# Kernel tuning notes

Measured on AMD Instinct MI355X. Metric: run time of the kernel, lower is better.

Reference implementation:

```python
import jax, jax.numpy as jnp
import numpy as np
import math

EMBED_DIM = 512
NUM_HEADS = 8
NUM_EXPERTS = 16
TOP_K = 8
B, T = 2, 1024


def setup_inputs() -> dict:
    key = jax.random.key(0)
    ks = jax.random.split(key, 16)
    d, E = EMBED_DIM, NUM_EXPERTS
    hdim = 4 * d  # expert hidden width
    s = 0.02
    inp = {
        "x": jax.random.normal(ks[0], (B, T, d), jnp.float32),
        # RMSNorm params (init ones, matching torch module)
        "g": jnp.ones((d,), jnp.float32),
        "b": jnp.ones((d,), jnp.float32),
        # attention
        "c_attn_w": jax.random.normal(ks[1], (d, 3 * d), jnp.float32) * s,
        "c_attn_b": jnp.zeros((3 * d,), jnp.float32),
        "alpha": jnp.ones((NUM_HEADS,), jnp.float32),
        "c_proj_w": jax.random.normal(ks[2], (d, d), jnp.float32) * s,
        "c_proj_b": jnp.zeros((d,), jnp.float32),
        # router
        "router_w": jax.random.normal(ks[3], (d, E), jnp.float32) * s,
        "router_b": jnp.zeros((E,), jnp.float32),
        # stacked expert params: Linear(d,4d) -> SwiGLU(4d,4d) -> Linear(4d,d)
        "w_in": jax.random.normal(ks[4], (E, d, hdim), jnp.float32) * s,
        "b_in": jnp.zeros((E, hdim), jnp.float32),
        "w1": jax.random.normal(ks[5], (E, hdim, 2 * hdim), jnp.float32) * s,
        "b1": jnp.zeros((E, 2 * hdim), jnp.float32),
        "w2": jax.random.normal(ks[6], (E, hdim, hdim), jnp.float32) * s,
        "b2": jnp.zeros((E, hdim), jnp.float32),
        "w_out": jax.random.normal(ks[7], (E, hdim, d), jnp.float32) * s,
        "b_out": jnp.zeros((E, d), jnp.float32),
    }
    return inp


def _block(x, g, b, c_attn_w, c_attn_b, alpha, c_proj_w, c_proj_b,
           router_w, router_b, w_in, b_in, w1, b1, w2, b2, w_out, b_out):
    Bb, Tt, C = x.shape
    H = alpha.shape[0]
    hd = C // H
    E = router_b.shape[0]

    # RMSNorm (note: additive b, per original module)
    rms = jnp.sqrt(jnp.mean(x * x, axis=-1, keepdims=True) + 1e-6)
    xn = (x / rms) * g + b

    # QK-normalized causal attention
    qkv = xn @ c_attn_w + c_attn_b                      # [B,T,3C]
    q, k, v = jnp.split(qkv, 3, axis=-1)
    def heads(t):
        return t.reshape(Bb, Tt, H, hd).transpose(0, 2, 1, 3)  # [B,H,T,hd]
    q, k, v = heads(q), heads(k), heads(v)
    eps = 1e-5
    q_hat = q / (jnp.linalg.norm(q, axis=-1, keepdims=True) + eps)
    k_hat = k / (jnp.linalg.norm(k, axis=-1, keepdims=True) + eps)
    factor = (alpha * math.sqrt(hd)).reshape(1, H, 1, 1)
    q_scaled = q_hat * factor
    # SDPA default scale = 1/sqrt(head_dim)
    scores = jnp.einsum("bhqd,bhkd->bhqk", q_scaled, k_hat) / math.sqrt(hd)
    causal = jnp.tril(jnp.ones((Tt, Tt), bool))
    scores = jnp.where(causal, scores, -jnp.inf)
    att = jax.nn.softmax(scores, axis=-1)
    y = jnp.einsum("bhqk,bhkd->bhqd", att, v)
    y = y.transpose(0, 2, 1, 3).reshape(Bb, Tt, C)
    y = y @ c_proj_w + c_proj_b
    x = x + y

    # Router + top-8 normalized gates
    routes = jax.nn.softmax(x @ router_w + router_b, axis=-1)  # [B,T,E]
    probs, idx = jax.lax.top_k(routes, TOP_K)
    probs = probs / jnp.sum(probs, axis=-1, keepdims=True)
    # combine weights per expert: [B,T,E]
    gates = jnp.sum(jax.nn.one_hot(idx, E, dtype=x.dtype) * probs[..., None], axis=2)

    # Dense expert evaluation (faithful math: unselected tokens get zero gate)
    N = Bb * Tt
    xf = x.reshape(N, C)
    gf = gates.reshape(N, E)
    h = jnp.einsum("nd,edf->enf", xf, w_in) + b_in[:, None, :]      # [E,N,4d]
    c = jnp.einsum("enf,efg->eng", h, w1) + b1[:, None, :]          # [E,N,8d]
    a, bb2 = jnp.split(c, 2, axis=-1)
    s = (bb2 * jax.nn.sigmoid(bb2)) * a                              # SwiGLU
    o = jnp.einsum("enf,efg->eng", s, w2) + b2[:, None, :]          # [E,N,4d]
    eo = jnp.einsum("enf,efd->end", o, w_out) + b_out[:, None, :]   # [E,N,d]
    moe = jnp.einsum("end,ne->nd", eo, gf).reshape(Bb, Tt, C)
    return x + moe


def reference(x, g, b, c_attn_w, c_attn_b, alpha, c_proj_w, c_proj_b,
              router_w, router_b, w_in, b_in, w1, b1, w2, b2, w_out, b_out):
    return _block(x, g, b, c_attn_w, c_attn_b, alpha, c_proj_w, c_proj_b,
                  router_w, router_b, w_in, b_in, w1, b1, w2, b2, w_out, b_out)
```

## Files before the change

kernel.cpp:

```cpp
#include <hip/hip_runtime.h>
#include <stdint.h>

#define DEVI __device__ __forceinline__
#define FENCE() asm volatile("" ::: "memory")

typedef short short8 __attribute__((ext_vector_type(8)));
typedef short short4v __attribute__((ext_vector_type(4)));
typedef float f32x4 __attribute__((ext_vector_type(4)));

DEVI float bf2f(unsigned short s){ union{unsigned u; float f;} x; x.u = ((unsigned)s)<<16; return x.f; }
DEVI unsigned short f2bf(float f){ union{float f; unsigned u;} x; x.f=f; unsigned r = x.u + 0x7fff + ((x.u>>16)&1); return (unsigned short)(r>>16); }

DEVI void gload_lds16(const void* g, void* l){
  __builtin_amdgcn_global_load_lds((const __attribute__((address_space(1))) unsigned int*)g,
                                   (__attribute__((address_space(3))) unsigned int*)l, 16, 0, 0);
}

__global__ __launch_bounds__(256)
void transpose_cvt(const float* __restrict__ in, unsigned short* __restrict__ out, int K, int N)
{
  __shared__ float tile[32][33];
  size_t zoff = (size_t)blockIdx.z * K * N;
  const float* src = in + zoff;
  unsigned short* dst = out + zoff;
  int kb = blockIdx.y*32, nb = blockIdx.x*32;
  int t = threadIdx.x;
  int tr = t>>3, tc = (t&7)*4;
  float4 v = *(const float4*)(src + (size_t)(kb+tr)*N + nb + tc);
  tile[tr][tc+0]=v.x; tile[tr][tc+1]=v.y; tile[tr][tc+2]=v.z; tile[tr][tc+3]=v.w;
  __syncthreads();
  short4v ov;
  ov[0] = (short)f2bf(tile[tc+0][tr]);
  ov[1] = (short)f2bf(tile[tc+1][tr]);
  ov[2] = (short)f2bf(tile[tc+2][tr]);
  ov[3] = (short)f2bf(tile[tc+3][tr]);
  *(short4v*)(dst + (size_t)(nb+tr)*K + kb + tc) = ov;
}

__global__ __launch_bounds__(256)
void rmsnorm_k(const float* __restrict__ x, const float* __restrict__ gw,
               const float* __restrict__ bw, unsigned short* __restrict__ xn)
{
  int row = blockIdx.x*4 + (threadIdx.x>>6);
  int lane = threadIdx.x & 63;
  const float* xr = x + (size_t)row*512 + lane*8;
  float4 a = *(const float4*)xr;
  float4 c = *(const float4*)(xr+4);
  float ss = a.x*a.x+a.y*a.y+a.z*a.z+a.w*a.w + c.x*c.x+c.y*c.y+c.z*c.z+c.w*c.w;
  #pragma unroll
  for (int m=1;m<64;m<<=1) ss += __shfl_xor(ss, m);
  float inv = 1.0f / sqrtf(ss*(1.f/512.f) + 1e-6f);
  const float* gr = gw + lane*8; const float* br = bw + lane*8;
  float4 g0=*(const float4*)gr, g1=*(const float4*)(gr+4);
  float4 b0=*(const float4*)br, b1=*(const float4*)(br+4);
  short8 o;
  o[0]=(short)f2bf(a.x*inv*g0.x + b0.x);
  o[1]=(short)f2bf(a.y*inv*g0.y + b0.y);
  o[2]=(short)f2bf(a.z*inv*g0.z + b0.z);
  o[3]=(short)f2bf(a.w*inv*g0.w + b0.w);
  o[4]=(short)f2bf(c.x*inv*g1.x + b1.x);
  o[5]=(short)f2bf(c.y*inv*g1.y + b1.y);
  o[6]=(short)f2bf(c.z*inv*g1.z + b1.z);
  o[7]=(short)f2bf(c.w*inv*g1.w + b1.w);
  *(short8*)(xn + (size_t)row*512 + lane*8) = o;
}

template<int EPI>
__global__ __launch_bounds__(512, 2)
void gemm3(const unsigned short* __restrict__ A, const unsigned short* __restrict__ B,
           const float* __restrict__ bias,
           float* __restrict__ Cf, unsigned short* __restrict__ Ch,
           const unsigned short* __restrict__ aux,
           int M, int N, int K,
           const int* __restrict__ off, long long strideBz, long long strideBiasz)
{
  __shared__ char smem[147456];
  int z = blockIdx.z;
  int rowbase = 0, Mz = M;
  if (off){ rowbase = off[z]; Mz = off[z+1] - rowbase; }
  int row0 = blockIdx.y * 256;
  if (row0 >= Mz) return;
  int col0 = blockIdx.x * 128;
  const unsigned short* Ab = A + (size_t)(rowbase + row0) * K;
  const unsigned short* Bb = B + (size_t)z * strideBz + (size_t)col0 * K;
  const float* biasz = bias + (size_t)z * strideBiasz;

  int tid = threadIdx.x;
  int lane = tid & 63, w = tid >> 6;
  int lrow = lane & 15, lg = lane >> 4;
  int wr = w >> 1, wc = w & 1;

  f32x4 acc[4][4];
  #pragma unroll
  for (int i=0;i<4;i++){
    #pragma unroll
    for (int j=0;j<4;j++) acc[i][j] = f32x4{0.f,0.f,0.f,0.f};
  }

  int nkt = K >> 6;

  auto stage = [&](int kt2, int part){
    if (kt2 >= nkt) return;
    char* sA = smem + (kt2 % 3) * 49152;
    char* sB = sA + 32768;
    int k0 = kt2 << 6;
    #pragma unroll
    for (int i=0;i<2;i++){
      int s = (part*2 + i)*512 + tid;
      int r = s >> 3, kb = (s & 7) ^ (r & 7);
      gload_lds16(Ab + (size_t)r*K + k0 + kb*8, sA + s*16);
    }
    {
      int s = part*512 + tid;
      int r = s >> 3, kb = (s & 7) ^ (r & 7);
      gload_lds16(Bb + (size_t)r*K + k0 + kb*8, sB + s*16);
    }
  };

  stage(0,0); stage(0,1); stage(1,0); stage(1,1);
  asm volatile("s_waitcnt vmcnt(6)" ::: "memory");
  __builtin_amdgcn_s_barrier();
  FENCE();

  for (int kt = 0; kt < nkt; kt++){
    char* sA = smem + (kt % 3) * 49152;
    char* sB = sA + 32768;
    short8 bfr[4][2], afr[4][2];
    #pragma unroll
    for (int n=0;n<4;n++){
      int ct = wc*64 + n*16 + lrow;
      #pragma unroll
      for (int kk=0;kk<2;kk++){
        int kbb = lg + kk*4;
        bfr[n][kk] = *(const short8*)(sB + ct*128 + ((kbb ^ (ct&7))<<4));
      }
    }
    #pragma unroll
    for (int m=0;m<2;m++){
      int rt = wr*64 + m*16 + lrow;
      #pragma unroll
      for (int kk=0;kk<2;kk++){
        int kbb = lg + kk*4;
        afr[m][kk] = *(const short8*)(sA + rt*128 + ((kbb ^ (rt&7))<<4));
      }
    }
    stage(kt+2, 0);
    FENCE(); __builtin_amdgcn_s_barrier(); FENCE();
    __builtin_amdgcn_s_setprio(1);
    #pragma unroll
    for (int m=0;m<2;m++){
      #pragma unroll
      for (int n=0;n<4;n++){
        #pragma unroll
        for (int kk=0;kk<2;kk++)
          acc[m][n] = __builtin_amdgcn_mfma_f32_16x16x32_bf16(afr[m][kk], bfr[n][kk], acc[m][n], 0,0,0);
      }
    }
    __builtin_amdgcn_s_setprio(0);
    FENCE(); __builtin_amdgcn_s_barrier(); FENCE();
    #pragma unroll
    for (int m=2;m<4;m++){
      int rt = wr*64 + m*16 + lrow;
      #pragma unroll
      for (int kk=0;kk<2;kk++){
        int kbb = lg + kk*4;
        afr[m][kk] = *(const short8*)(sA + rt*128 + ((kbb ^ (rt&7))<<4));
      }
    }
    stage(kt+2, 1);
    FENCE(); __builtin_amdgcn_s_barrier(); FENCE();
    __builtin_amdgcn_s_setprio(1);
    #pragma unroll
    for (int m=2;m<4;m++){
      #pragma unroll
      for (int n=0;n<4;n++){
        #pragma unroll
        for (int kk=0;kk<2;kk++)
          acc[m][n] = __builtin_amdgcn_mfma_f32_16x16x32_bf16(afr[m][kk], bfr[n][kk], acc[m][n], 0,0,0);
      }
    }
    __builtin_amdgcn_s_setprio(0);
    asm volatile("s_waitcnt vmcnt(6)" ::: "memory");
    FENCE(); __builtin_amdgcn_s_barrier(); FENCE();
  }

  #pragma unroll
  for (int m=0;m<4;m++){
    int rloc = wr*64 + m*16 + lg*4;
    #pragma unroll
    for (int j=0;j<4;j++){
      int row = row0 + rloc + j;
      if (row < Mz){
        size_t rg = (size_t)(rowbase + row);
        #pragma unroll
        for (int n=0;n<4;n++){
          int col = col0 + wc*64 + n*16 + lrow;
          float v = acc[m][n][j] + biasz[col];
          size_t idx = rg * N + col;
          if constexpr (EPI == 0){
            Cf[idx] = v;
          } else if constexpr (EPI == 1){
            Ch[idx] = f2bf(v);
          } else {
            float a = bf2f(aux[idx]);
            float sg = v / (1.f + __expf(-v));
            Ch[idx] = f2bf(a * sg);
          }
        }
      }
    }
  }
}

__global__ __launch_bounds__(256)
void gemm_proj(const unsigned short* __restrict__ A, const unsigned short* __restrict__ B,
               const float* __restrict__ bias,
               float* __restrict__ Cf, unsigned short* __restrict__ Ch,
               const float* __restrict__ resid, int M, int N, int K)
{
  __shared__ char smem[32768];
  char* smA = smem; char* smB = smem + 16384;
  int row0 = blockIdx.y * 128;
  int col0 = blockIdx.x * 128;
  int t = threadIdx.x, w = t>>6, lane = t&63;
  int lrow = lane&15, lg = lane>>4;
  int wr = w>>1, wc = w&1;

  f32x4 acc[4][4];
  #pragma unroll
  for (int i=0;i<4;i++){
    #pragma unroll
    for (int j=0;j<4;j++) acc[i][j] = f32x4{0.f,0.f,0.f,0.f};
  }
  const size_t Abase = (size_t)row0 * K;
  const size_t Bbase = (size_t)col0 * K;
  int nkt = K >> 6;
  for (int kt=0; kt<nkt; kt++){
    __syncthreads();
    int k0 = kt*64;
    #pragma unroll
    for (int i=0;i<4;i++){
      int s = (i*4 + w)*64 + lane;
      int r = s>>3;
      int kb = (s&7) ^ (r&7);
      gload_lds16(A + Abase + (size_t)r*K + k0 + kb*8, smA + (size_t)(i*4+w)*1024);
      gload_lds16(B + Bbase + (size_t)r*K + k0 + kb*8, smB + (size_t)(i*4+w)*1024);
    }
    __syncthreads();
    #pragma unroll
    for (int ks=0; ks<2; ks++){
      short8 af[4], bf[4];
      int kbb = lg + ks*4;
      #pragma unroll
      for (int m=0;m<4;m++){
        int rt = wr*64 + m*16 + lrow;
        af[m] = *(const short8*)(smA + rt*128 + ((kbb ^ (rt&7))<<4));
      }
      #pragma unroll
      for (int n=0;n<4;n++){
        int rt = wc*64 + n*16 + lrow;
        bf[n] = *(const short8*)(smB + rt*128 + ((kbb ^ (rt&7))<<4));
      }
      #pragma unroll
      for (int m=0;m<4;m++){
        #pragma unroll
        for (int n=0;n<4;n++)
          acc[m][n] = __builtin_amdgcn_mfma_f32_16x16x32_bf16(af[m], bf[n], acc[m][n], 0,0,0);
      }
    }
  }
  #pragma unroll
  for (int m=0;m<4;m++){
    int rloc = wr*64 + m*16 + lg*4;
    #pragma unroll
    for (int j=0;j<4;j++){
      int row = row0 + rloc + j;
      size_t rg = (size_t)row;
      #pragma unroll
      for (int n=0;n<4;n++){
        int col = col0 + wc*64 + n*16 + lrow;
        float v = acc[m][n][j] + bias[col];
        size_t idx = rg * N + col;
        v += resid[idx];
        Cf[idx] = v;
        Ch[idx] = f2bf(v);
      }
    }
  }
}

__global__ __launch_bounds__(256)
void prep_qkv(const float* __restrict__ qkv, const float* __restrict__ alpha,
              unsigned short* __restrict__ q_s, unsigned short* __restrict__ k_hat,
              unsigned short* __restrict__ v_t)
{
  int idx = blockIdx.x*4 + (threadIdx.x>>6);
  int lane = threadIdx.x & 63;
  int h = idx & 7, bt = idx >> 3;
  size_t base = (size_t)bt*1536 + h*64 + lane;
  float qv = qkv[base], kv = qkv[base+512], vv = qkv[base+1024];
  float qs2 = qv*qv, ks2 = kv*kv;
  #pragma unroll
  for (int m=1;m<64;m<<=1){ qs2 += __shfl_xor(qs2, m); ks2 += __shfl_xor(ks2, m); }
  float qh = qv / (sqrtf(qs2) + 1e-5f) * alpha[h];
  float kh = kv / (sqrtf(ks2) + 1e-5f);
  int b = bt >> 10, tt = bt & 1023;
  size_t hb = ((size_t)(b*8+h))*1024*64;
  q_s[hb + (size_t)tt*64 + lane] = f2bf(qh);
  k_hat[hb + (size_t)tt*64 + lane] = f2bf(kh);
  v_t[((size_t)(b*8+h)*64 + lane)*1024 + tt] = f2bf(vv);
}

__global__ __launch_bounds__(256)
void attn_k(const unsigned short* __restrict__ q_s, const unsigned short* __restrict__ k_hat,
            const unsigned short* __restrict__ v_t, unsigned short* __restrict__ y)
{
  __shared__ char sm[51200];
  char* smK = sm + 18432;
  char* smV = sm + 34816;
  int qt = blockIdx.x, bh = blockIdx.y;
  int b = bh>>3, h = bh&7;
  int t = threadIdx.x, w = t>>6, lane = t&63;
  int lrow = lane&15, lg = lane>>4;
  int q0 = qt*128;
  const size_t hQK = (size_t)bh*1024*64;
  const size_t hV  = (size_t)bh*64*1024;

  #pragma unroll
  for (int i=0;i<4;i++){
    int s = (i*4+w)*64 + lane;
    int r = s>>3, kb = (s&7)^(r&7);
    gload_lds16(q_s + hQK + (size_t)(q0+r)*64 + kb*8, sm + (size_t)(i*4+w)*1024);
  }
  __syncthreads();
  short8 qf[2][2];
  #pragma unroll
  for (int mf=0;mf<2;mf++){
    #pragma unroll
    for (int ks=0;ks<2;ks++){
      int rt = w*32 + mf*16 + lrow;
      int kbb = lg + ks*4;
      qf[mf][ks] = *(const short8*)(sm + rt*128 + ((kbb^(rt&7))<<4));
    }
  }
  f32x4 oacc[2][4];
  #pragma unroll
  for (int i=0;i<2;i++){
    #pragma unroll
    for (int j=0;j<4;j++) oacc[i][j] = f32x4{0.f,0.f,0.f,0.f};
  }
  float mrun[2][4], lrun[2][4];
  #pragma unroll
  for (int i=0;i<2;i++){
    #pragma unroll
    for (int j=0;j<4;j++){ mrun[i][j] = -1e30f; lrun[i][j] = 0.f; }
  }
  char* Pw = sm + w*4608;

  for (int kt=0; kt<=qt; kt++){
    __syncthreads();
    int t0 = kt*128;
    #pragma unroll
    for (int i=0;i<4;i++){
      int s = (i*4+w)*64 + lane;
      int r = s>>3, kb = (s&7)^(r&7);
      gload_lds16(k_hat + hQK + (size_t)(t0+r)*64 + kb*8, smK + (size_t)(i*4+w)*1024);
    }
    #pragma unroll
    for (int i=0;i<4;i++){
      int s = (i*4+w)*64 + lane;
      int d = s>>4, kb2 = s&15;
      int kb = kb2 ^ (d&7);
      gload_lds16(v_t + hV + (size_t)d*1024 + t0 + kb*8, smV + (size_t)(i*4+w)*1024);
    }
    __syncthreads();

    f32x4 sacc[2][8];
    #pragma unroll
    for (int i=0;i<2;i++){
      #pragma unroll
      for (int j=0;j<8;j++) sacc[i][j] = f32x4{0.f,0.f,0.f,0.f};
    }
    #pragma unroll
    for (int ks=0;ks<2;ks++){
      short8 kf[8];
      int kbb = lg + ks*4;
      #pragma unroll
      for (int nf=0;nf<8;nf++){
        int rt = nf*16+lrow;
        kf[nf] = *(const short8*)(smK + rt*128 + ((kbb^(rt&7))<<4));
      }
      #pragma unroll
      for (int mf=0;mf<2;mf++){
        #pragma unroll
        for (int nf=0;nf<8;nf++)
          sacc[mf][nf] = __builtin_amdgcn_mfma_f32_16x16x32_bf16(qf[mf][ks], kf[nf], sacc[mf][nf], 0,0,0);
      }
    }
    if (kt == qt){
      #pragma unroll
      for (int mf=0;mf<2;mf++){
        #pragma unroll
        for (int nf=0;nf<8;nf++){
          #pragma unroll
          for (int j=0;j<4;j++){
            int qi = w*32+mf*16+lg*4+j;
            int ki = nf*16 + lrow;
            if (ki > qi) sacc[mf][nf][j] = -1e30f;
          }
        }
      }
    }
    #pragma unroll
    for (int mf=0;mf<2;mf++){
      #pragma unroll
      for (int j=0;j<4;j++){
        float mx = sacc[mf][0][j];
        #pragma unroll
        for (int nf=1;nf<8;nf++) mx = fmaxf(mx, sacc[mf][nf][j]);
        #pragma unroll
        for (int m=1;m<16;m<<=1) mx = fmaxf(mx, __shfl_xor(mx, m));
        float mnew = fmaxf(mrun[mf][j], mx);
        float sc = __expf(mrun[mf][j] - mnew);
        float rs = 0.f;
        #pragma unroll
        for (int nf=0;nf<8;nf++){
          float p = __expf(sacc[mf][nf][j] - mnew);
          sacc[mf][nf][j] = p; rs += p;
        }
        #pragma unroll
        for (int m=1;m<16;m<<=1) rs += __shfl_xor(rs, m);
        lrun[mf][j] = lrun[mf][j]*sc + rs;
        mrun[mf][j] = mnew;
        #pragma unroll
        for (int n2=0;n2<4;n2++) oacc[mf][n2][j] *= sc;
      }
    }
    #pragma unroll
    for (int half=0; half<2; half++){
      #pragma unroll
      for (int mf=0;mf<2;mf++){
        #pragma unroll
        for (int nfh=0;nfh<4;nfh++){
          int nf = half*4 + nfh;
          #pragma unroll
          for (int j=0;j<4;j++){
            int row = mf*16 + lg*4 + j;
            int col = nfh*16 + lrow;
            *(unsigned short*)(Pw + (row*72 + col)*2) = f2bf(sacc[mf][nf][j]);
          }
        }
      }
      #pragma unroll
      for (int k2=0;k2<2;k2++){
        int ks2 = half*2 + k2;
        short8 pf[2], vf[4];
        #pragma unroll
        for (int mf=0;mf<2;mf++)
          pf[mf] = *(const short8*)(Pw + (mf*16+lrow)*144 + lg*16 + k2*64);
        #pragma unroll
        for (int n2=0;n2<4;n2++){
          int d = n2*16+lrow;
          int kbb2 = lg + ks2*4;
          vf[n2] = *(const short8*)(smV + d*256 + ((kbb2^(d&7))<<4));
        }
        #pragma unroll
        for (int mf=0;mf<2;mf++){
          #pragma unroll
          for (int n2=0;n2<4;n2++)
            oacc[mf][n2] = __builtin_amdgcn_mfma_f32_16x16x32_bf16(pf[mf], vf[n2], oacc[mf][n2], 0,0,0);
        }
      }
    }
  }
  #pragma unroll
  for (int mf=0;mf<2;mf++){
    #pragma unroll
    for (int n2=0;n2<4;n2++){
      #pragma unroll
      for (int j=0;j<4;j++){
        float v = oacc[mf][n2][j] / lrun[mf][j];
        int qi = q0 + w*32 + mf*16 + lg*4 + j;
        int d = n2*16 + lrow;
        y[((size_t)(b*1024+qi))*512 + h*64 + d] = f2bf(v);
      }
    }
  }
}

__global__ __launch_bounds__(256)
void router_topk(const float* __restrict__ x2f, const float* __restrict__ rw,
                 const float* __restrict__ rb, float* __restrict__ gates)
{
  int tkn = blockIdx.x*4 + (threadIdx.x>>6);
  int lane = threadIdx.x & 63;
  int e = lane & 15, p = lane >> 4;
  const float* xr = x2f + (size_t)tkn*512;
  float part = 0.f;
  for (int d = p*128; d < p*128+128; d++)
    part += xr[d] * rw[d*16 + e];
  part += __shfl_xor(part, 16);
  part += __shfl_xor(part, 32);
  float logit = part + rb[e];
  float mx = logit;
  #pragma unroll
  for (int m=1;m<16;m<<=1) mx = fmaxf(mx, __shfl_xor(mx, m));
  float ex = __expf(logit - mx);
  float sm = ex;
  #pragma unroll
  for (int m=1;m<16;m<<=1) sm += __shfl_xor(sm, m);
  float prob = ex / sm;
  bool taken = false;
  float ssum = 0.f;
  #pragma unroll
  for (int r=0;r<8;r++){
    float cv = taken ? -1.f : prob;
    int ci = e;
    #pragma unroll
    for (int m=1;m<16;m<<=1){
      float ov = __shfl_xor(cv, m);
      int oi = __shfl_xor(ci, m);
      if (ov > cv || (ov == cv && oi < ci)){ cv = ov; ci = oi; }
    }
    if (e == ci) taken = true;
    ssum += cv;
  }
  if (lane < 16)
    gates[(size_t)tkn*16 + e] = taken ? prob / ssum : 0.f;
}

__global__ void listbuild(const float* __restrict__ gates, int* __restrict__ list,
                          int* __restrict__ slot, int* __restrict__ cnt)
{
  int e = blockIdx.x;
  int tid = threadIdx.x, w = tid>>6, lane = tid&63;
  __shared__ int sbase;
  __shared__ int wsum[4];
  if (tid==0) sbase = 0;
  __syncthreads();
  for (int c=0;c<8;c++){
    int tk = c*256 + tid;
    bool flag = gates[(size_t)tk*16 + e] > 0.f;
    unsigned long long bal = __ballot(flag);
    if (lane==0) wsum[w] = (int)__popcll(bal);
    __syncthreads();
    int wpref = 0;
    for (int i=0;i<w;i++) wpref += wsum[i];
    int tot = wsum[0]+wsum[1]+wsum[2]+wsum[3];
    int lpref = (int)__popcll(bal & ((1ull<<lane)-1ull));
    if (flag){
      int pos = sbase + wpref + lpref;
      list[e*2048 + pos] = tk;
      slot[(size_t)tk*16 + e] = pos;
    }
    __syncthreads();
    if (tid==0) sbase += tot;
    __syncthreads();
  }
  if (tid==0) cnt[e] = sbase;
}

__global__ void prefix_off(const int* __restrict__ cnt, int* __restrict__ off){
  if (threadIdx.x==0 && blockIdx.x==0){
    int a=0;
    for (int e=0;e<16;e++){ off[e]=a; a+=cnt[e]; }
    off[16]=a;
  }
}

__global__ __launch_bounds__(256)
void gather_rows(const unsigned short* __restrict__ x2h, const int* __restrict__ list,
                 const int* __restrict__ cnt, const int* __restrict__ off,
                 unsigned short* __restrict__ xe)
{
  int e = blockIdx.y;
  int s = blockIdx.x*4 + (threadIdx.x>>6);
  if (s >= cnt[e]) return;
  int lane = threadIdx.x & 63;
  int tk = list[e*2048 + s];
  *(short8*)(xe + ((size_t)(off[e]+s))*512 + lane*8) =
      *(const short8*)(x2h + (size_t)tk*512 + lane*8);
}

__global__ __launch_bounds__(256)
void combine_k(const float* __restrict__ x2f, const unsigned short* __restrict__ eo,
               const float* __restrict__ gates, const int* __restrict__ slot,
               const int* __restrict__ off, float* __restrict__ out)
{
  int tkn = blockIdx.x;
  __shared__ float gs[16];
  __shared__ int rws[16];
  int tid = threadIdx.x;
  if (tid < 16){
    float g = gates[(size_t)tkn*16 + tid];
    gs[tid] = g;
    rws[tid] = (g > 0.f) ? (off[tid] + slot[(size_t)tkn*16 + tid]) : 0;
  }
  __syncthreads();
  for (int d = tid; d < 512; d += 256){
    float v = x2f[(size_t)tkn*512 + d];
    #pragma unroll
    for (int e=0;e<16;e++){
      float g = gs[e];
      if (g > 0.f) v += g * bf2f(eo[(size_t)rws[e]*512 + d]);
    }
    out[(size_t)tkn*512 + d] = v;
  }
}

extern "C" void kernel_launch(void* const* d_in, const int* in_sizes, int n_in,
                              void* d_out, int out_size, void* d_ws, size_t ws_size,
                              hipStream_t stream) {
  (void)in_sizes; (void)n_in; (void)out_size; (void)ws_size;
  const float* x    = (const float*)d_in[0];
  const float* gw   = (const float*)d_in[1];
  const float* bw   = (const float*)d_in[2];
  const float* caw  = (const float*)d_in[3];
  const float* cab  = (const float*)d_in[4];
  const float* alpha= (const float*)d_in[5];
  const float* cpw  = (const float*)d_in[6];
  const float* cpb  = (const float*)d_in[7];
  const float* rw   = (const float*)d_in[8];
  const float* rb   = (const float*)d_in[9];
  const float* w_in = (const float*)d_in[10];
  const float* b_in = (const float*)d_in[11];
  const float* w1   = (const float*)d_in[12];
  const float* b1   = (const float*)d_in[13];
  const float* w2   = (const float*)d_in[14];
  const float* b2   = (const float*)d_in[15];
  const float* w_out= (const float*)d_in[16];
  const float* b_out= (const float*)d_in[17];

  char* ws = (char*)d_ws;
  size_t o = 0;
  auto alloc = [&](size_t bytes)->char*{
    char* p = ws + o;
    o += (bytes + 255) & ~(size_t)255;
    return p;
  };
  const size_t PADROWS = 16896;
  unsigned short* wT_attn = (unsigned short*)alloc(1536ull*512*2);
  unsigned short* wT_proj = (unsigned short*)alloc(512ull*512*2);
  unsigned short* wT_in   = (unsigned short*)alloc(16ull*2048*512*2);
  unsigned short* wT_1    = (unsigned short*)alloc(16ull*4096*2048*2);
  unsigned short* wT_2    = (unsigned short*)alloc(16ull*2048*2048*2);
  unsigned short* wT_out  = (unsigned short*)alloc(16ull*512*2048*2);
  unsigned short* xn      = (unsigned short*)alloc(2048ull*512*2);
  float*          qkv     = (float*)alloc(2048ull*1536*4);
  unsigned short* q_s     = (unsigned short*)alloc(2048ull*512*2);
  unsigned short* k_hat   = (unsigned short*)alloc(2048ull*512*2);
  unsigned short* v_t     = (unsigned short*)alloc(2048ull*512*2);
  unsigned short* ybuf    = (unsigned short*)alloc(2048ull*512*2);
  float*          x2f     = (float*)alloc(2048ull*512*4);
  unsigned short* x2h     = (unsigned short*)alloc(2048ull*512*2);
  float*          gates   = (float*)alloc(2048ull*16*4);
  int*            slot    = (int*)alloc(2048ull*16*4);
  int*            list    = (int*)alloc(16ull*2048*4);
  int*            cnt     = (int*)alloc(64);
  int*            off     = (int*)alloc(256);
  unsigned short* xe      = (unsigned short*)alloc(PADROWS*512*2);
  unsigned short* hbuf    = (unsigned short*)alloc(PADROWS*2048*2);
  unsigned short* c1buf   = (unsigned short*)alloc(PADROWS*2048*2);
  unsigned short* sbuf    = (unsigned short*)alloc(PADROWS*2048*2);
  unsigned short* eobuf   = xe;
  unsigned short* obuf    = hbuf;

  dim3 blk(256);
  dim3 blk5(512);
  transpose_cvt<<<dim3(1536/32, 512/32, 1), blk, 0, stream>>>(caw, wT_attn, 512, 1536);
  transpose_cvt<<<dim3(512/32, 512/32, 1), blk, 0, stream>>>(cpw, wT_proj, 512, 512);
  transpose_cvt<<<dim3(2048/32, 512/32, 16), blk, 0, stream>>>(w_in, wT_in, 512, 2048);
  transpose_cvt<<<dim3(4096/32, 2048/32, 16), blk, 0, stream>>>(w1, wT_1, 2048, 4096);
  transpose_cvt<<<dim3(2048/32, 2048/32, 16), blk, 0, stream>>>(w2, wT_2, 2048, 2048);
  transpose_cvt<<<dim3(512/32, 2048/32, 16), blk, 0, stream>>>(w_out, wT_out, 2048, 512);

  rmsnorm_k<<<512, blk, 0, stream>>>(x, gw, bw, xn);
  gemm3<0><<<dim3(12, 8, 1), blk5, 0, stream>>>(xn, wT_attn, cab, qkv, nullptr, nullptr,
                                                2048, 1536, 512, nullptr, 0, 0);
  prep_qkv<<<4096, blk, 0, stream>>>(qkv, alpha, q_s, k_hat, v_t);
  attn_k<<<dim3(8,16), blk, 0, stream>>>(q_s, k_hat, v_t, ybuf);
  gemm_proj<<<dim3(4,16,1), blk, 0, stream>>>(ybuf, wT_proj, cpb, x2f, x2h, x, 2048, 512, 512);
  router_topk<<<512, blk, 0, stream>>>(x2f, rw, rb, gates);
  listbuild<<<16, blk, 0, stream>>>(gates, list, slot, cnt);
  prefix_off<<<1, 64, 0, stream>>>(cnt, off);
  gather_rows<<<dim3(512,16), blk, 0, stream>>>(x2h, list, cnt, off, xe);

  gemm3<1><<<dim3(16,8,16), blk5, 0, stream>>>(xe, wT_in, b_in, nullptr, hbuf, nullptr,
                                               0, 2048, 512, off, 2048ll*512, 2048);
  gemm3<1><<<dim3(16,8,16), blk5, 0, stream>>>(hbuf, wT_1, b1, nullptr, c1buf, nullptr,
                                               0, 2048, 2048, off, 4096ll*2048, 4096);
  gemm3<2><<<dim3(16,8,16), blk5, 0, stream>>>(hbuf, wT_1 + 2048ull*2048, b1 + 2048, nullptr, sbuf,
                                               c1buf, 0, 2048, 2048, off, 4096ll*2048, 4096);
  gemm3<1><<<dim3(16,8,16), blk5, 0, stream>>>(sbuf, wT_2, b2, nullptr, obuf, nullptr,
                                               0, 2048, 2048, off, 2048ll*2048, 2048);
  gemm3<1><<<dim3(4,8,16), blk5, 0, stream>>>(obuf, wT_out, b_out, nullptr, eobuf, nullptr,
                                              0, 512, 2048, off, 512ll*2048, 512);
  combine_k<<<2048, blk, 0, stream>>>(x2f, eobuf, gates, slot, off, (float*)d_out);
}
```

Baseline: 1.173 ms.

## Fuse SwiGLU gate/value GEMMs via interleaved w1, swizzle blocks, smaller attention tiles

Interleaves w1 columns during the transpose so each 32-column group holds 16 value and 16 gate columns. This lets one GEMM compute both halves and apply SwiGLU in its epilogue, removing the c1buf intermediate write and read and one launch. It also remaps GEMM block indices with an XCD-aware swizzle, drains outstanding loads on the last iterations, and halves the attention query tile to 64 rows to double the grid. The trade-off is extra index arithmetic and a more complex weight layout.

New measurement: 1.187 ms. No clear change (+1.2%).

```diff
diff --git a/kernel.cpp b/kernel.cpp
--- a/kernel.cpp
+++ b/kernel.cpp
@@ -38,6 +38,30 @@
 }
 
 __global__ __launch_bounds__(256)
+void transpose_cvt_w1(const float* __restrict__ w1, unsigned short* __restrict__ outp)
+{
+  __shared__ float tile[32][33];
+  int e = blockIdx.z;
+  const float* src = w1 + (size_t)e*2048*4096;
+  unsigned short* dst = outp + (size_t)e*4096*2048;
+  int np0 = blockIdx.x*32;
+  int k0 = blockIdx.y*32;
+  int g = np0 >> 5;
+  int t = threadIdx.x;
+  int tr = t>>3, tc = (t&7)*4;
+  int srccol = (tc < 16) ? (g*16 + tc) : (2048 + g*16 + (tc-16));
+  float4 v = *(const float4*)(src + (size_t)(k0+tr)*4096 + srccol);
+  tile[tr][tc+0]=v.x; tile[tr][tc+1]=v.y; tile[tr][tc+2]=v.z; tile[tr][tc+3]=v.w;
+  __syncthreads();
+  short4v ov;
+  ov[0] = (short)f2bf(tile[tc+0][tr]);
+  ov[1] = (short)f2bf(tile[tc+1][tr]);
+  ov[2] = (short)f2bf(tile[tc+2][tr]);
+  ov[3] = (short)f2bf(tile[tc+3][tr]);
+  *(short4v*)(dst + (size_t)(np0+tr)*2048 + k0 + tc) = ov;
+}
+
+__global__ __launch_bounds__(256)
 void rmsnorm_k(const float* __restrict__ x, const float* __restrict__ gw,
                const float* __restrict__ bw, unsigned short* __restrict__ xn)
 {
@@ -70,17 +94,24 @@
 void gemm3(const unsigned short* __restrict__ A, const unsigned short* __restrict__ B,
            const float* __restrict__ bias,
            float* __restrict__ Cf, unsigned short* __restrict__ Ch,
-           const unsigned short* __restrict__ aux,
            int M, int N, int K,
            const int* __restrict__ off, long long strideBz, long long strideBiasz)
 {
   __shared__ char smem[147456];
-  int z = blockIdx.z;
+  int nbx = gridDim.x, nby = gridDim.y;
+  int pl = nbx*nby;
+  int lin = ((int)blockIdx.z*nby + (int)blockIdx.y)*nbx + (int)blockIdx.x;
+  int nwg = pl*(int)gridDim.z;
+  int cpx = nwg >> 3;
+  int swz = (lin & 7)*cpx + (lin >> 3);
+  int z  = swz / pl; int rxy = swz - z*pl;
+  int by = rxy / nbx; int bx = rxy - by*nbx;
+
   int rowbase = 0, Mz = M;
   if (off){ rowbase = off[z]; Mz = off[z+1] - rowbase; }
-  int row0 = blockIdx.y * 256;
+  int row0 = by * 256;
   if (row0 >= Mz) return;
-  int col0 = blockIdx.x * 128;
+  int col0 = bx * 128;
   const unsigned short* Ab = A + (size_t)(rowbase + row0) * K;
   const unsigned short* Bb = B + (size_t)z * strideBz + (size_t)col0 * K;
   const float* biasz = bias + (size_t)z * strideBiasz;
@@ -180,7 +211,8 @@
       }
     }
     __builtin_amdgcn_s_setprio(0);
-    asm volatile("s_waitcnt vmcnt(6)" ::: "memory");
+    if (kt + 2 < nkt) { asm volatile("s_waitcnt vmcnt(6)" ::: "memory"); }
+    else              { asm volatile("s_waitcnt vmcnt(0)" ::: "memory"); }
     FENCE(); __builtin_amdgcn_s_barrier(); FENCE();
   }
 
@@ -192,19 +224,24 @@
       int row = row0 + rloc + j;
       if (row < Mz){
         size_t rg = (size_t)(rowbase + row);
-        #pragma unroll
-        for (int n=0;n<4;n++){
-          int col = col0 + wc*64 + n*16 + lrow;
-          float v = acc[m][n][j] + biasz[col];
-          size_t idx = rg * N + col;
-          if constexpr (EPI == 0){
-            Cf[idx] = v;
-          } else if constexpr (EPI == 1){
-            Ch[idx] = f2bf(v);
-          } else {
-            float a = bf2f(aux[idx]);
-            float sg = v / (1.f + __expf(-v));
-            Ch[idx] = f2bf(a * sg);
+        if constexpr (EPI == 2){
+          #pragma unroll
+          for (int nf=0;nf<4;nf+=2){
+            int pcol = col0 + wc*64 + nf*16;
+            int scol = ((pcol>>5)<<4) + lrow;
+            float av = acc[m][nf][j]   + biasz[scol];
+            float gv = acc[m][nf+1][j] + biasz[2048 + scol];
+            float sg = gv / (1.f + __expf(-gv));
+            Ch[rg*2048 + scol] = f2bf(av * sg);
+          }
+        } else {
+          #pragma unroll
+          for (int n=0;n<4;n++){
+            int col = col0 + wc*64 + n*16 + lrow;
+            float v = acc[m][n][j] + biasz[col];
+            size_t idx = rg * N + col;
+            if constexpr (EPI == 0) Cf[idx] = v;
+            else                    Ch[idx] = f2bf(v);
           }
         }
       }
@@ -322,42 +359,34 @@
   int b = bh>>3, h = bh&7;
   int t = threadIdx.x, w = t>>6, lane = t&63;
   int lrow = lane&15, lg = lane>>4;
-  int q0 = qt*128;
+  int q0 = qt*64;
   const size_t hQK = (size_t)bh*1024*64;
   const size_t hV  = (size_t)bh*64*1024;
 
   #pragma unroll
-  for (int i=0;i<4;i++){
-    int s = (i*4+w)*64 + lane;
-    int r = s>>3, kb = (s&7)^(r&7);
-    gload_lds16(q_s + hQK + (size_t)(q0+r)*64 + kb*8, sm + (size_t)(i*4+w)*1024);
+  for (int i=0;i<2;i++){
+    int si = i*256 + t;
+    int r = si>>3, kb = (si&7)^(r&7);
+    gload_lds16(q_s + hQK + (size_t)(q0+r)*64 + kb*8, sm + (size_t)si*16);
   }
   __syncthreads();
-  short8 qf[2][2];
-  #pragma unroll
-  for (int mf=0;mf<2;mf++){
-    #pragma unroll
-    for (int ks=0;ks<2;ks++){
-      int rt = w*32 + mf*16 + lrow;
-      int kbb = lg + ks*4;
-      qf[mf][ks] = *(const short8*)(sm + rt*128 + ((kbb^(rt&7))<<4));
-    }
-  }
-  f32x4 oacc[2][4];
-  #pragma unroll
-  for (int i=0;i<2;i++){
-    #pragma unroll
-    for (int j=0;j<4;j++) oacc[i][j] = f32x4{0.f,0.f,0.f,0.f};
-  }
-  float mrun[2][4], lrun[2][4];
-  #pragma unroll
-  for (int i=0;i<2;i++){
-    #pragma unroll
-    for (int j=0;j<4;j++){ mrun[i][j] = -1e30f; lrun[i][j] = 0.f; }
-  }
-  char* Pw = sm + w*4608;
-
-  for (int kt=0; kt<=qt; kt++){
+  short8 qf[2];
+  #pragma unroll
+  for (int ks=0;ks<2;ks++){
+    int rt = w*16 + lrow;
+    int kbb = lg + ks*4;
+    qf[ks] = *(const short8*)(sm + rt*128 + ((kbb^(rt&7))<<4));
+  }
+  f32x4 oacc[4];
+  #pragma unroll
+  for (int j=0;j<4;j++) oacc[j] = f32x4{0.f,0.f,0.f,0.f};
+  float mrun[4], lrun[4];
+  #pragma unroll
+  for (int j=0;j<4;j++){ mrun[j] = -1e30f; lrun[j] = 0.f; }
+  char* Pw = sm + w*2304;
+
+  int ktmax = (q0 + 63) >> 7;
+  for (int kt=0; kt<=ktmax; kt++){
     __syncthreads();
     int t0 = kt*128;
     #pragma unroll
@@ -375,12 +404,9 @@
     }
     __syncthreads();
 
-    f32x4 sacc[2][8];
-    #pragma unroll
-    for (int i=0;i<2;i++){
-      #pragma unroll
-      for (int j=0;j<8;j++) sacc[i][j] = f32x4{0.f,0.f,0.f,0.f};
-    }
+    f32x4 sacc[8];
+    #pragma unroll
+    for (int j=0;j<8;j++) sacc[j] = f32x4{0.f,0.f,0.f,0.f};
     #pragma unroll
     for (int ks=0;ks<2;ks++){
       short8 kf[8];
@@ -391,73 +417,59 @@
         kf[nf] = *(const short8*)(smK + rt*128 + ((kbb^(rt&7))<<4));
       }
       #pragma unroll
-      for (int mf=0;mf<2;mf++){
+      for (int nf=0;nf<8;nf++)
+        sacc[nf] = __builtin_amdgcn_mfma_f32_16x16x32_bf16(qf[ks], kf[nf], sacc[nf], 0,0,0);
+    }
+    if (kt == ktmax){
+      #pragma unroll
+      for (int nf=0;nf<8;nf++){
         #pragma unroll
-        for (int nf=0;nf<8;nf++)
-          sacc[mf][nf] = __builtin_amdgcn_mfma_f32_16x16x32_bf16(qf[mf][ks], kf[nf], sacc[mf][nf], 0,0,0);
-      }
-    }
-    if (kt == qt){
-      #pragma unroll
-      for (int mf=0;mf<2;mf++){
+        for (int j=0;j<4;j++){
+          int qi = q0 + w*16 + lg*4 + j;
+          int ki = t0 + nf*16 + lrow;
+          if (ki > qi) sacc[nf][j] = -1e30f;
+        }
+      }
+    }
+    #pragma unroll
+    for (int j=0;j<4;j++){
+      float mx = sacc[0][j];
+      #pragma unroll
+      for (int nf=1;nf<8;nf++) mx = fmaxf(mx, sacc[nf][j]);
+      #pragma unroll
+      for (int m=1;m<16;m<<=1) mx = fmaxf(mx, __shfl_xor(mx, m));
+      float mnew = fmaxf(mrun[j], mx);
+      float sc = __expf(mrun[j] - mnew);
+      float rs = 0.f;
+      #pragma unroll
+      for (int nf=0;nf<8;nf++){
+        float p = __expf(sacc[nf][j] - mnew);
+        sacc[nf][j] = p; rs += p;
+      }
+      #pragma unroll
+      for (int m=1;m<16;m<<=1) rs += __shfl_xor(rs, m);
+      lrun[j] = lrun[j]*sc + rs;
+      mrun[j] = mnew;
+      #pragma unroll
+      for (int n2=0;n2<4;n2++) oacc[n2][j] *= sc;
+    }
+    #pragma unroll
+    for (int half=0; half<2; half++){
+      #pragma unroll
+      for (int nfh=0;nfh<4;nfh++){
+        int nf = half*4 + nfh;
         #pragma unroll
-        for (int nf=0;nf<8;nf++){
-          #pragma unroll
-          for (int j=0;j<4;j++){
-            int qi = w*32+mf*16+lg*4+j;
-            int ki = nf*16 + lrow;
-            if (ki > qi) sacc[mf][nf][j] = -1e30f;
-          }
-        }
-      }
-    }
-    #pragma unroll
-    for (int mf=0;mf<2;mf++){
-      #pragma unroll
-      for (int j=0;j<4;j++){
-        float mx = sacc[mf][0][j];
-        #pragma unroll
-        for (int nf=1;nf<8;nf++) mx = fmaxf(mx, sacc[mf][nf][j]);
-        #pragma unroll
-        for (int m=1;m<16;m<<=1) mx = fmaxf(mx, __shfl_xor(mx, m));
-        float mnew = fmaxf(mrun[mf][j], mx);
-        float sc = __expf(mrun[mf][j] - mnew);
-        float rs = 0.f;
-        #pragma unroll
-        for (int nf=0;nf<8;nf++){
-          float p = __expf(sacc[mf][nf][j] - mnew);
-          sacc[mf][nf][j] = p; rs += p;
-        }
-        #pragma unroll
-        for (int m=1;m<16;m<<=1) rs += __shfl_xor(rs, m);
-        lrun[mf][j] = lrun[mf][j]*sc + rs;
-        mrun[mf][j] = mnew;
-        #pragma unroll
-        for (int n2=0;n2<4;n2++) oacc[mf][n2][j] *= sc;
-      }
-    }
-    #pragma unroll
-    for (int half=0; half<2; half++){
-      #pragma unroll
-      for (int mf=0;mf<2;mf++){
-        #pragma unroll
-        for (int nfh=0;nfh<4;nfh++){
-          int nf = half*4 + nfh;
-          #pragma unroll
-          for (int j=0;j<4;j++){
-            int row = mf*16 + lg*4 + j;
-            int col = nfh*16 + lrow;
-            *(unsigned short*)(Pw + (row*72 + col)*2) = f2bf(sacc[mf][nf][j]);
-          }
+        for (int j=0;j<4;j++){
+          int row = lg*4 + j;
+          int col = nfh*16 + lrow;
+          *(unsigned short*)(Pw + (row*72 + col)*2) = f2bf(sacc[nf][j]);
         }
       }
       #pragma unroll
       for (int k2=0;k2<2;k2++){
         int ks2 = half*2 + k2;
-        short8 pf[2], vf[4];
-        #pragma unroll
-        for (int mf=0;mf<2;mf++)
-          pf[mf] = *(const short8*)(Pw + (mf*16+lrow)*144 + lg*16 + k2*64);
+        short8 pf, vf[4];
+        pf = *(const short8*)(Pw + lrow*144 + lg*16 + k2*64);
         #pragma unroll
         for (int n2=0;n2<4;n2++){
           int d = n2*16+lrow;
@@ -465,25 +477,19 @@
           vf[n2] = *(const short8*)(smV + d*256 + ((kbb2^(d&7))<<4));
         }
         #pragma unroll
-        for (int mf=0;mf<2;mf++){
-          #pragma unroll
-          for (int n2=0;n2<4;n2++)
-            oacc[mf][n2] = __builtin_amdgcn_mfma_f32_16x16x32_bf16(pf[mf], vf[n2], oacc[mf][n2], 0,0,0);
-        }
-      }
-    }
-  }
-  #pragma unroll
-  for (int mf=0;mf<2;mf++){
-    #pragma unroll
-    for (int n2=0;n2<4;n2++){
-      #pragma unroll
-      for (int j=0;j<4;j++){
-        float v = oacc[mf][n2][j] / lrun[mf][j];
-        int qi = q0 + w*32 + mf*16 + lg*4 + j;
-        int d = n2*16 + lrow;
-        y[((size_t)(b*1024+qi))*512 + h*64 + d] = f2bf(v);
-      }
+        for (int n2=0;n2<4;n2++)
+          oacc[n2] = __builtin_amdgcn_mfma_f32_16x16x32_bf16(pf, vf[n2], oacc[n2], 0,0,0);
+      }
+    }
+  }
+  #pragma unroll
+  for (int n2=0;n2<4;n2++){
+    #pragma unroll
+    for (int j=0;j<4;j++){
+      float v = oacc[n2][j] / lrun[j];
+      int qi = q0 + w*16 + lg*4 + j;
+      int d = n2*16 + lrow;
+      y[((size_t)(b*1024+qi))*512 + h*64 + d] = f2bf(v);
     }
   }
 }
@@ -642,7 +648,7 @@
   unsigned short* wT_attn = (unsigned short*)alloc(1536ull*512*2);
   unsigned short* wT_proj = (unsigned short*)alloc(512ull*512*2);
   unsigned short* wT_in   = (unsigned short*)alloc(16ull*2048*512*2);
-  unsigned short* wT_1    = (unsigned short*)alloc(16ull*4096*2048*2);
+  unsigned short* wT1p    = (unsigned short*)alloc(16ull*4096*2048*2);
   unsigned short* wT_2    = (unsigned short*)alloc(16ull*2048*2048*2);
   unsigned short* wT_out  = (unsigned short*)alloc(16ull*512*2048*2);
   unsigned short* xn      = (unsigned short*)alloc(2048ull*512*2);
@@ -660,7 +666,6 @@
   int*            off     = (int*)alloc(256);
   unsigned short* xe      = (unsigned short*)alloc(PADROWS*512*2);
   unsigned short* hbuf    = (unsigned short*)alloc(PADROWS*2048*2);
-  unsigned short* c1buf   = (unsigned short*)alloc(PADROWS*2048*2);
   unsigned short* sbuf    = (unsigned short*)alloc(PADROWS*2048*2);
   unsigned short* eobuf   = xe;
   unsigned short* obuf    = hbuf;
@@ -670,30 +675,28 @@
   transpose_cvt<<<dim3(1536/32, 512/32, 1), blk, 0, stream>>>(caw, wT_attn, 512, 1536);
   transpose_cvt<<<dim3(512/32, 512/32, 1), blk, 0, stream>>>(cpw, wT_proj, 512, 512);
   transpose_cvt<<<dim3(2048/32, 512/32, 16), blk, 0, stream>>>(w_in, wT_in, 512, 2048);
-  transpose_cvt<<<dim3(4096/32, 2048/32, 16), blk, 0, stream>>>(w1, wT_1, 2048, 4096);
+  transpose_cvt_w1<<<dim3(4096/32, 2048/32, 16), blk, 0, stream>>>(w1, wT1p);
   transpose_cvt<<<dim3(2048/32, 2048/32, 16), blk, 0, stream>>>(w2, wT_2, 2048, 2048);
   transpose_cvt<<<dim3(512/32, 2048/32, 16), blk, 0, stream>>>(w_out, wT_out, 2048, 512);
 
   rmsnorm_k<<<512, blk, 0, stream>>>(x, gw, bw, xn);
-  gemm3<0><<<dim3(12, 8, 1), blk5, 0, stream>>>(xn, wT_attn, cab, qkv, nullptr, nullptr,
+  gemm3<0><<<dim3(12, 8, 1), blk5, 0, stream>>>(xn, wT_attn, cab, qkv, nullptr,
                                                 2048, 1536, 512, nullptr, 0, 0);
   prep_qkv<<<4096, blk, 0, stream>>>(qkv, alpha, q_s, k_hat, v_t);
-  attn_k<<<dim3(8,16), blk, 0, stream>>>(q_s, k_hat, v_t, ybuf);
+  attn_k<<<dim3(16,16), blk, 0, stream>>>(q_s, k_hat, v_t, ybuf);
   gemm_proj<<<dim3(4,16,1), blk, 0, stream>>>(ybuf, wT_proj, cpb, x2f, x2h, x, 2048, 512, 512);
   router_topk<<<512, blk, 0, stream>>>(x2f, rw, rb, gates);
   listbuild<<<16, blk, 0, stream>>>(gates, list, slot, cnt);
   prefix_off<<<1, 64, 0, stream>>>(cnt, off);
   gather_rows<<<dim3(512,16), blk, 0, stream>>>(x2h, list, cnt, off, xe);
 
-  gemm3<1><<<dim3(16,8,16), blk5, 0, stream>>>(xe, wT_in, b_in, nullptr, hbuf, nullptr,
+  gemm3<1><<<dim3(16,8,16), blk5, 0, stream>>>(xe, wT_in, b_in, nullptr, hbuf,
                                                0, 2048, 512, off, 2048ll*512, 2048);
-  gemm3<1><<<dim3(16,8,16), blk5, 0, stream>>>(hbuf, wT_1, b1, nullptr, c1buf, nullptr,
-                                               0, 2048, 2048, off, 4096ll*2048, 4096);
-  gemm3<2><<<dim3(16,8,16), blk5, 0, stream>>>(hbuf, wT_1 + 2048ull*2048, b1 + 2048, nullptr, sbuf,
-                                               c1buf, 0, 2048, 2048, off, 4096ll*2048, 4096);
-  gemm3<1><<<dim3(16,8,16), blk5, 0, stream>>>(sbuf, wT_2, b2, nullptr, obuf, nullptr,
+  gemm3<2><<<dim3(32,8,16), blk5, 0, stream>>>(hbuf, wT1p, b1, nullptr, sbuf,
+                                               0, 4096, 2048, off, 4096ll*2048, 4096);
+  gemm3<1><<<dim3(16,8,16), blk5, 0, stream>>>(sbuf, wT_2, b2, nullptr, obuf,
                                                0, 2048, 2048, off, 2048ll*2048, 2048);
-  gemm3<1><<<dim3(4,8,16), blk5, 0, stream>>>(obuf, wT_out, b_out, nullptr, eobuf, nullptr,
+  gemm3<1><<<dim3(4,8,16), blk5, 0, stream>>>(obuf, wT_out, b_out, nullptr, eobuf,
                                               0, 512, 2048, off, 512ll*2048, 512);
   combine_k<<<2048, blk, 0, stream>>>(x2f, eobuf, gates, slot, off, (float*)d_out);
 }
```
